# Performance work log

Hardware: AMD Instinct MI355X
Metric: run time of the kernel (lower is better)

The kernel has to match this reference:

```python
import jax, jax.numpy as jnp
import numpy as np
from jax.scipy.linalg import expm

B, Q, F, R, T, H = 2048, 16, 512, 400, 50, 256
STEPS = 100
DT = 1.0 / STEPS
COH = 50.0  # coherence_time


def setup_inputs() -> dict:
    ks = jax.random.split(jax.random.key(0), 48)
    it = iter(range(48))
    def rn(shape, s=1.0):
        return jax.random.normal(ks[next(it)], shape, dtype=jnp.float32) * s
    A = rn((Q, Q)); Bm = rn((Q, Q))
    d = {
        'molecular_features': rn((B, F)),
        'noise': rn((B, T, R), 0.1),          # torch.randn_like * 0.1
        'amp_re': rn((B, Q)), 'amp_im': rn((B, Q)),
        'H_re': (A + A.T) / 2.0,               # hermitized: real part symmetric
        'H_im': (Bm - Bm.T) / 2.0,             # imag part antisymmetric
        'gpc': rn((R,)),
        'bw1': rn((256, Q + F), (Q + F) ** -0.5), 'bb1': rn((256,), 0.01),
        'bw2': rn((128, 256), 256 ** -0.5), 'bb2': rn((128,), 0.01),
        'bw3': rn((R, 128), 128 ** -0.5), 'bb3': rn((R,), 0.01),
    }
    ins = [R, H, H]
    for l in range(3):
        d[f'Wih{l}'] = rn((4 * H, ins[l]), ins[l] ** -0.5)
        d[f'Whh{l}'] = rn((4 * H, H), H ** -0.5)
        d[f'bih{l}'] = rn((4 * H,), 0.01)
        d[f'bhh{l}'] = rn((4 * H,), 0.01)
    d.update({
        'cw1': rn((512, H + R), (H + R) ** -0.5), 'cb1': rn((512,), 0.01),
        'cw2': rn((256, 512), 512 ** -0.5), 'cb2': rn((256,), 0.01),
        'cw3': rn((64, 256), 256 ** -0.5), 'cb3': rn((64,), 0.01),
        'cw4': rn((1, 64), 64 ** -0.5), 'cb4': rn((1,), 0.01),
    })
    return d


def _lstm_layer(x, Wih, Whh, bih, bhh):
    # PyTorch LSTM gate order: i, f, g, o
    def step(carry, xt):
        h, c = carry
        z = xt @ Wih.T + h @ Whh.T + bih + bhh
        ig, fg, gg, og = jnp.split(z, 4, axis=-1)
        c = jax.nn.sigmoid(fg) * c + jax.nn.sigmoid(ig) * jnp.tanh(gg)
        h = jax.nn.sigmoid(og) * jnp.tanh(c)
        return (h, c), h
    n = x.shape[0]
    init = (jnp.zeros((n, H), x.dtype), jnp.zeros((n, H), x.dtype))
    (hT, _), hs = jax.lax.scan(step, init, jnp.swapaxes(x, 0, 1))
    return jnp.swapaxes(hs, 0, 1), hT


def _forward(molecular_features, noise, amp_re, amp_im, H_re, H_im, gpc,
             bw1, bb1, bw2, bb2, bw3, bb3,
             Wih0, Whh0, bih0, bhh0, Wih1, Whh1, bih1, bhh1, Wih2, Whh2, bih2, bhh2,
             cw1, cb1, cw2, cb2, cw3, cb3, cw4, cb4):
    Hp = (H_re + 1j * H_im).astype(jnp.complex64)
    amp = (amp_re + 1j * amp_im).astype(jnp.complex64)
    amp = amp / jnp.linalg.norm(amp, axis=-1, keepdims=True)  # F.normalize
    # molecular interaction Hamiltonian (real part only, as in source)
    M = jnp.einsum('bi,ij->bij', molecular_features[:, :Q], H_re)
    def qstep(a, step):
        t = step * DT
        Ht = Hp[None, :, :] + M * t                 # [B,Q,Q] complex
        U = jax.vmap(expm)(-1j * Ht * DT)           # per-sample matrix_exp
        a = jnp.einsum('bij,bj->bi', U, a) * jnp.exp(-t / COH)
        return a, None
    amp, _ = jax.lax.scan(qstep, amp, jnp.arange(STEPS, dtype=jnp.float32))
    obs = (jnp.abs(amp) ** 2).astype(jnp.float32)   # quantum observables
    bio = jnp.concatenate([obs, molecular_features], axis=-1)  # [B, Q+F]
    h1 = jax.nn.relu(bio @ bw1.T + bb1)
    h2 = jnp.tanh(h1 @ bw2.T + bb2)
    receptor = jax.nn.sigmoid(h2 @ bw3.T + bb3)     # [B, R]
    # biological signal transduction
    g_amp = receptor * jax.nn.sigmoid(gpc)
    adapt = jnp.exp(-jnp.arange(T, dtype=jnp.float32) / 10.0)[None, :, None]
    seq = g_amp[:, None, :] * adapt + noise         # [B, T, R]
    x, hT = _lstm_layer(seq, Wih0, Whh0, bih0, bhh0)
    x, hT = _lstm_layer(x, Wih1, Whh1, bih1, bhh1)
    x, hT = _lstm_layer(x, Wih2, Whh2, bih2, bhh2)  # hT: last-layer hidden [B,H]
    cf = jnp.concatenate([hT, receptor], axis=-1)   # [B, H+R]
    c1 = jax.nn.relu(cf @ cw1.T + cb1)
    c2 = jax.nn.relu(c1 @ cw2.T + cb2)
    c3 = jnp.tanh(c2 @ cw3.T + cb3)
    cons = jnp.mean(jax.nn.sigmoid(c3 @ cw4.T + cb4))
    valence = jnp.mean(jnp.tanh(x), axis=(1, 2))    # [B]
    return receptor, x, valence, cons, amp


def reference(molecular_features, noise, amp_re, amp_im, H_re, H_im, gpc,
              bw1, bb1, bw2, bb2, bw3, bb3,
              Wih0, Whh0, bih0, bhh0, Wih1, Whh1, bih1, bhh1, Wih2, Whh2, bih2, bhh2,
              cw1, cb1, cw2, cb2, cw3, cb3, cw4, cb4):
    receptor, seq, valence, cons, amp = _forward(
        molecular_features, noise, amp_re, amp_im, H_re, H_im, gpc,
        bw1, bb1, bw2, bb2, bw3, bb3,
        Wih0, Whh0, bih0, bhh0, Wih1, Whh1, bih1, bhh1, Wih2, Whh2, bih2, bhh2,
        cw1, cb1, cw2, cb2, cw3, cb3, cw4, cb4)
    # von Neumann entanglement entropy across a 2/2 qubit bipartition (Q=16 -> 4x4)
    half = 2 ** ((int(np.log2(Q))) // 2)
    rs = amp.reshape(amp.shape[0], half, -1)
    rho = jnp.einsum('bij,bik->bjk', rs, jnp.conj(rs))
    ev = jnp.clip(jnp.linalg.eigvals(rho).real, 1e-12, None)
    ent = jnp.mean(-jnp.sum(ev * jnp.log(ev), axis=-1))
    return receptor, seq, valence, cons, ent
```

## Files before the change

kernel.cpp:

```cpp
#include <hip/hip_runtime.h>
#include <stdint.h>


using short8 = __attribute__((ext_vector_type(8))) short;
using f32x4  = __attribute__((ext_vector_type(4))) float;

#define DEV static __device__ __forceinline__

typedef const __attribute__((address_space(1))) void GV;
typedef __attribute__((address_space(3))) void LV;
DEV void gload16(const void* g, void* l) {
  __builtin_amdgcn_global_load_lds((GV*)g, (LV*)l, 16, 0, 0);
}

DEV ushort f2b(float x) {
  union { float f; uint32_t u; } v; v.f = x;
  uint32_t r = v.u + 0x7FFFu + ((v.u >> 16) & 1u);
  return (ushort)(r >> 16);
}
DEV float b2f(ushort x) {
  union { uint32_t u; float f; } v; v.u = ((uint32_t)x) << 16; return v.f;
}
DEV float sigf(float x) { return 1.f / (1.f + __expf(-x)); }
DEV float tanh_fast(float x) {
  float xc = fminf(9.f, fmaxf(-9.f, x));
  float e = __expf(2.f * xc);
  return (e - 1.f) / (e + 1.f);
}

struct CJob { const float* src; ushort* dst; const float* scale;
              long n; int sr, sc, dc, mode; };
struct CJobs { CJob j[13]; };

__global__ __launch_bounds__(256)
void k_convbatch(CJobs jobs) {
  const int job = blockIdx.x >> 8;
  const int blk = blockIdx.x & 255;
  const CJob J = jobs.j[job];
  for (long idx = (long)blk * 256 + threadIdx.x; idx < J.n; idx += 256L * 256) {
    int r = (int)(idx / J.dc), c = (int)(idx % J.dc);
    float v = 0.f;
    if (r < J.sr && c < J.sc) {
      v = J.src[(long)r * J.sc + c];
      if (J.mode == 1) v *= sigf(J.scale[c]);
    }
    J.dst[idx] = f2b(v);
  }
}

__global__ __launch_bounds__(256)
void k_vadd3(const float* a0, const float* b0, const float* a1, const float* b1,
             const float* a2, const float* b2, float* o) {
  const int job = blockIdx.x >> 2;
  const int i = (blockIdx.x & 3) * 256 + threadIdx.x;
  const float* a = (job == 0) ? a0 : (job == 1) ? a1 : a2;
  const float* b = (job == 0) ? b0 : (job == 1) ? b1 : b2;
  o[job * 1024 + i] = a[i] + b[i];
}

__global__ __launch_bounds__(256)
void k_qb(const float* __restrict__ ampr_in, const float* __restrict__ ampi_in,
          const float* __restrict__ Hre, const float* __restrict__ Him,
          const float* __restrict__ mf, ushort* __restrict__ bio,
          float* __restrict__ ampr_out, float* __restrict__ ampi_out) {
  const int tid = threadIdx.x;
  if (blockIdx.x < 256) {
    const int gid = blockIdx.x * 256 + tid;
    const int b = gid >> 5;
    const int l32 = gid & 31;
    const int i = l32 & 15;
    const int h = l32 >> 4;
    float hre[8], him[8];
#pragma unroll
    for (int jj = 0; jj < 8; jj++) {
      hre[jj] = Hre[i * 16 + h * 8 + jj];
      him[jj] = Him[i * 16 + h * 8 + jj];
    }
    const float mfi = mf[(long)b * 512 + i];
    float are = ampr_in[b * 16 + i], aim = ampi_in[b * 16 + i];
    float ss = are * are + aim * aim;
#pragma unroll
    for (int m = 1; m < 32; m <<= 1) ss += __shfl_xor(ss, m, 32);
    ss *= 0.5f;
    const float inv = 1.f / sqrtf(ss);
    are *= inv; aim *= inv;
#pragma unroll 1
    for (int st = 0; st < 100; ++st) {
      const float t = (float)st * 0.01f;
      const float fac = 1.f + t * mfi;
      const float dec = __expf(-t * 0.02f);
      float tre = are, tim = aim, rre = are, rim = aim;
#pragma unroll 1
      for (int k = 1; k <= 5; k++) {
        float w1r = 0.f, w1i = 0.f, w2r = 0.f, w2i = 0.f;
#pragma unroll
        for (int jj = 0; jj < 8; jj++) {
          const float vr = __shfl(tre, h * 8 + jj, 32);
          const float vi = __shfl(tim, h * 8 + jj, 32);
          w1r += hre[jj] * vr; w1i += hre[jj] * vi;
          w2r += him[jj] * vr; w2i += him[jj] * vi;
        }
        w1r += __shfl_xor(w1r, 16, 32);
        w1i += __shfl_xor(w1i, 16, 32);
        w2r += __shfl_xor(w2r, 16, 32);
        w2i += __shfl_xor(w2i, 16, 32);
        const float hr = w1r * fac - w2i;
        const float hi = w1i * fac + w2r;
        const float sk = 0.01f / (float)k;
        tre = sk * hi; tim = -sk * hr;
        rre += tre; rim += tim;
      }
      are = rre * dec; aim = rim * dec;
    }
    if (h == 0) {
      ampr_out[b * 16 + i] = are;
      ampi_out[b * 16 + i] = aim;
      bio[(long)b * 576 + i] = f2b(are * are + aim * aim);
    }
  } else {
    for (long i = (long)(blockIdx.x - 256) * 256 + tid; i < (long)2048 * 512;
         i += 2048L * 256) {
      long b = i >> 9, k = i & 511;
      bio[b * 576 + 16 + k] = f2b(mf[i]);
    }
  }
}

template<int BT>
__global__ __launch_bounds__(256)
void k_gemm(const ushort* __restrict__ A, int lda,
            const ushort* __restrict__ W, int ldw,
            const float* __restrict__ bias,
            const ushort* __restrict__ Gg, int t0,
            float* __restrict__ Cf, int ldcf,
            ushort* __restrict__ Cb, int ldcb,
            int N, int K, int act, int swz) {
  constexpr int FR = BT / 32;
  constexpr int CH = BT / 32;
  __shared__ __align__(16) ushort lsA[2][BT * 64];
  __shared__ __align__(16) ushort lsB[2][BT * 64];
  const int tid = threadIdx.x;
  const int lane = tid & 63, w = tid >> 6;
  const int lr = lane & 15, lq = lane >> 4;
  const int wm = (w >> 1) * (BT / 2), wn = (w & 1) * (BT / 2);
  int bxb = blockIdx.x, byb = blockIdx.y;
  if (swz) {
    const int id = byb * gridDim.x + bxb;
    const int xcd = id & 7, q = id >> 3;
    byb = (q >> 4) * 16 + xcd * 2 + (q & 1);
    bxb = (q >> 1) & 7;
  }
  const int bm = byb * BT, bn = bxb * BT;
  const int srow = lane >> 3;
  const int scol = (((lane & 7) ^ srow)) * 8;

  auto stage = [&](int buf, int kk) {
#pragma unroll
    for (int c = 0; c < CH; c++) {
      const int ch = w * CH + c;
      const int r = ch * 8 + srow;
      gload16(A + (size_t)(bm + r) * lda + kk + scol, lsA[buf] + ch * 512);
      gload16(W + (size_t)(bn + r) * ldw + kk + scol, lsB[buf] + ch * 512);
    }
  };

  f32x4 acc[FR][FR];
#pragma unroll
  for (int i = 0; i < FR; i++)
#pragma unroll
    for (int j = 0; j < FR; j++) acc[i][j] = (f32x4){0.f, 0.f, 0.f, 0.f};

  stage(0, 0);
  __syncthreads();
  const int T = K >> 6;
  for (int t = 0; t < T; t++) {
    const int cur = t & 1;
    if (t + 1 < T) stage(cur ^ 1, (t + 1) * 64);
    short8 af[FR][2], bf[FR][2];
#pragma unroll
    for (int mi = 0; mi < FR; mi++)
#pragma unroll
      for (int k2 = 0; k2 < 2; k2++) {
        const int row = wm + mi * 16 + lr;
        af[mi][k2] = *(const short8*)(lsA[cur] + (row >> 3) * 512 + (row & 7) * 64 +
                                      (((k2 * 4 + lq) ^ (row & 7)) * 8));
      }
#pragma unroll
    for (int ni = 0; ni < FR; ni++)
#pragma unroll
      for (int k2 = 0; k2 < 2; k2++) {
        const int row = wn + ni * 16 + lr;
        bf[ni][k2] = *(const short8*)(lsB[cur] + (row >> 3) * 512 + (row & 7) * 64 +
                                      (((k2 * 4 + lq) ^ (row & 7)) * 8));
      }
#pragma unroll
    for (int k2 = 0; k2 < 2; k2++)
#pragma unroll
      for (int mi = 0; mi < FR; mi++)
#pragma unroll
        for (int ni = 0; ni < FR; ni++)
          acc[mi][ni] = __builtin_amdgcn_mfma_f32_16x16x32_bf16(
              af[mi][k2], bf[ni][k2], acc[mi][ni], 0, 0, 0);
    __syncthreads();
  }

#pragma unroll
  for (int mi = 0; mi < FR; mi++) {
#pragma unroll
    for (int r = 0; r < 4; r++) {
      const int row = bm + wm + mi * 16 + lq * 4 + r;
      float gfac = 0.f; const ushort* ggrow = nullptr;
      if (Gg) {
        gfac = __expf(-(float)(t0 + (row >> 11)) * 0.1f);
        ggrow = Gg + (size_t)(row & 2047) * 1024;
      }
#pragma unroll
      for (int ni = 0; ni < FR; ni++) {
        const int col = bn + wn + ni * 16 + lr;
        if (col < N) {
          float v = acc[mi][ni][r];
          if (bias) v += bias[col];
          if (Gg)  v += gfac * b2f(ggrow[col]);
          if (act == 1) v = fmaxf(v, 0.f);
          else if (act == 2) v = tanh_fast(v);
          else if (act == 3) v = sigf(v);
          if (Cf) Cf[(size_t)row * ldcf + col] = v;
          if (Cb) Cb[(size_t)row * ldcb + col] = f2b(v);
        }
      }
    }
  }
}

__global__ __launch_bounds__(512, 2)
void k_gemm8(const ushort* __restrict__ gA, int glda,
             const ushort* __restrict__ gW,
             const float* __restrict__ gbias, const ushort* __restrict__ gGg,
             int gt0, ushort* __restrict__ gC, int gK) {
  __shared__ __align__(16) ushort lsA[2 * 8192];
  __shared__ __align__(16) ushort lsB[2 * 8192];
  const int tid = threadIdx.x;
  const int gb = blockIdx.x;
  const int xcd = gb & 7, q = gb >> 3;
  const int byb = (q >> 4) * 16 + xcd * 2 + (q & 1);
  const int bxb = (q >> 1) & 7;
  const int bm = byb * 128, bn = bxb * 128;
  const int lane = tid & 63, wg = tid >> 6;
  const int lr = lane & 15, lq = lane >> 4;
  const int wm = (wg >> 2) * 64, wn = (wg & 3) * 32;
  const int srow = lane >> 3;
  const int scol = (((lane & 7) ^ srow)) * 8;

  f32x4 acc[4][2];
#pragma unroll
  for (int i = 0; i < 4; i++)
#pragma unroll
    for (int j = 0; j < 2; j++) acc[i][j] = (f32x4){0.f, 0.f, 0.f, 0.f};

#pragma unroll
  for (int c = 0; c < 2; c++) {
    const int ch = wg * 2 + c;
    const int r = ch * 8 + srow;
    gload16(gA + (size_t)(bm + r) * glda + scol, lsA + ch * 512);
    gload16(gW + (size_t)(bn + r) * glda + scol, lsB + ch * 512);
  }
  __syncthreads();

  const int T = gK >> 6;
  for (int t = 0; t < T; t++) {
    const int cur = t & 1;
    if (t + 1 < T) {
      const int kk = (t + 1) * 64;
#pragma unroll
      for (int c = 0; c < 2; c++) {
        const int ch = wg * 2 + c;
        const int r = ch * 8 + srow;
        gload16(gA + (size_t)(bm + r) * glda + kk + scol, lsA + (cur ^ 1) * 8192 + ch * 512);
        gload16(gW + (size_t)(bn + r) * glda + kk + scol, lsB + (cur ^ 1) * 8192 + ch * 512);
      }
    }
    {
      short8 af[4][2], bf[2][2];
#pragma unroll
      for (int mi = 0; mi < 4; mi++)
#pragma unroll
        for (int k2 = 0; k2 < 2; k2++) {
          const int row = wm + mi * 16 + lr;
          af[mi][k2] = *(const short8*)(lsA + cur * 8192 + (row >> 3) * 512 +
                                        (row & 7) * 64 + (((k2 * 4 + lq) ^ (row & 7)) * 8));
        }
#pragma unroll
      for (int ni = 0; ni < 2; ni++)
#pragma unroll
        for (int k2 = 0; k2 < 2; k2++) {
          const int row = wn + ni * 16 + lr;
          bf[ni][k2] = *(const short8*)(lsB + cur * 8192 + (row >> 3) * 512 +
                                        (row & 7) * 64 + (((k2 * 4 + lq) ^ (row & 7)) * 8));
        }
#pragma unroll
      for (int k2 = 0; k2 < 2; k2++)
#pragma unroll
        for (int mi = 0; mi < 4; mi++)
#pragma unroll
          for (int ni = 0; ni < 2; ni++)
            acc[mi][ni] = __builtin_amdgcn_mfma_f32_16x16x32_bf16(
                af[mi][k2], bf[ni][k2], acc[mi][ni], 0, 0, 0);
    }
    __syncthreads();
  }

#pragma unroll
  for (int mi = 0; mi < 4; mi++) {
#pragma unroll
    for (int r = 0; r < 4; r++) {
      const int row = bm + wm + mi * 16 + lq * 4 + r;
      float gfac = 0.f; const ushort* ggrow = nullptr;
      if (gGg) {
        gfac = __expf(-(float)(gt0 + (row >> 11)) * 0.1f);
        ggrow = gGg + (size_t)(row & 2047) * 1024;
      }
#pragma unroll
      for (int ni = 0; ni < 2; ni++) {
        const int col = bn + wn + ni * 16 + lr;
        float v = acc[mi][ni][r];
        if (gbias) v += gbias[col];
        if (gGg)  v += gfac * b2f(ggrow[col]);
        gC[(size_t)row * 1024 + col] = f2b(v);
      }
    }
  }
}

__global__ void k_noiseconv(const float* __restrict__ noise, ushort* __restrict__ dst, int t0) {
  long n = 10L * 2048 * 448;
  for (long idx = (long)blockIdx.x * blockDim.x + threadIdx.x; idx < n;
       idx += (long)gridDim.x * blockDim.x) {
    int r = (int)(idx % 448);
    long row = idx / 448;
    int b = (int)(row & 2047);
    int tl = (int)(row >> 11);
    ushort v = 0;
    if (r < 400)
      v = f2b(__builtin_nontemporal_load(&noise[((long)b * 50 + t0 + tl) * 400 + r]));
    dst[idx] = v;
  }
}

__global__ __launch_bounds__(512, 2)
void k_fused(const ushort* __restrict__ IH, const ushort* __restrict__ Whh,
             float* __restrict__ hstate, float* __restrict__ cstate,
             ushort* __restrict__ Hout, float* __restrict__ Xout, int t0,
             const ushort* __restrict__ gA, int glda,
             const ushort* __restrict__ gW,
             const float* __restrict__ gbias, const ushort* __restrict__ gGg,
             int gt0, ushort* __restrict__ gC, int gK) {
  __shared__ __align__(16) ushort upool[37024];
  const int tid = threadIdx.x;

  if (blockIdx.x < 128) {
    ushort (*h_lds)[266] = (ushort(*)[266])upool;
    ushort* ih0 = upool + 4256;
    const int lane = tid & 63, w8 = tid >> 6;
    const int lr = lane & 15, lq = lane >> 4;
    const int b0 = blockIdx.x * 16;
    const int wcols = w8 * 32;

    short8 wres[2][8];
#pragma unroll
    for (int cg = 0; cg < 2; cg++) {
      const ushort* wp = Whh + (size_t)(wcols + cg * 16 + lr) * 256 + lq * 8;
#pragma unroll
      for (int kk = 0; kk < 8; kk++) wres[cg][kk] = *(const short8*)(wp + kk * 32);
    }

    float c_reg[2][4], h_reg[2][4];
#pragma unroll
    for (int cg = 0; cg < 2; cg++) {
      const int j = wcols + cg * 16 + lr;
#pragma unroll
      for (int r = 0; r < 4; r++) {
        const int s = lq * 4 + r;
        float hv = hstate[(size_t)(b0 + s) * 256 + j];
        c_reg[cg][r] = cstate[(size_t)(b0 + s) * 256 + j];
        h_reg[cg][r] = hv;
        h_lds[s][j] = f2b(hv);
      }
    }
    __syncthreads();

#define LOADB(buf, g, cg) { \
  const ushort* wp_ = Whh + (size_t)((g) * 256 + wcols + (cg) * 16 + lr) * 256 + lq * 8; \
  _Pragma("unroll") for (int kk = 0; kk < 8; kk++) (buf)[kk] = *(const short8*)(wp_ + kk * 32); }
#define MFMAB(buf, g, cg) { \
  _Pragma("unroll") for (int kk = 0; kk < 8; kk++) \
    acc[cg][g] = __builtin_amdgcn_mfma_f32_16x16x32_bf16(af[kk], (buf)[kk], acc[cg][g], 0, 0, 0); }
#define MFMAR(cg) { \
  _Pragma("unroll") for (int kk = 0; kk < 8; kk++) \
    acc[cg][0] = __builtin_amdgcn_mfma_f32_16x16x32_bf16(af[kk], wres[cg][kk], acc[cg][0], 0, 0, 0); }

    for (int blk = 0; blk < 10; blk += 2) {
#pragma unroll
      for (int si = 0; si < 2; si++) {
        const ushort* src = IH + ((size_t)(blk + si) * 2048 + b0) * 1024;
#pragma unroll
        for (int u = 0; u < 4; u++) {
          const int bi = u * 8 + w8;
          gload16(src + (size_t)bi * 512 + lane * 8, ih0 + si * 16384 + bi * 512);
        }
      }
      __syncthreads();

      for (int i2 = 0; i2 < 2; i2++) {
        const int tl = blk + i2;
        const ushort* ihc = ih0 + i2 * 16384;
        short8 af[8];
#pragma unroll
        for (int kk = 0; kk < 8; kk++)
          af[kk] = *(const short8*)(&h_lds[lr][kk * 32 + lq * 8]);
        __syncthreads();

        f32x4 acc[2][4];
#pragma unroll
        for (int cg = 0; cg < 2; cg++)
#pragma unroll
          for (int g = 0; g < 4; g++) acc[cg][g] = (f32x4){0.f, 0.f, 0.f, 0.f};

        short8 wb0[8], wb1[8];
        LOADB(wb0, 1, 0);
        LOADB(wb1, 1, 1);
        MFMAR(0);
        MFMAR(1);
        MFMAB(wb0, 1, 0);
        LOADB(wb0, 2, 0);
        MFMAB(wb1, 1, 1);
        LOADB(wb1, 2, 1);
        MFMAB(wb0, 2, 0);
        LOADB(wb0, 3, 0);
        MFMAB(wb1, 2, 1);
        LOADB(wb1, 3, 1);
        MFMAB(wb0, 3, 0);
        MFMAB(wb1, 3, 1);

        const int t = t0 + tl;
#pragma unroll
        for (int cg = 0; cg < 2; cg++) {
          const int j = wcols + cg * 16 + lr;
#pragma unroll
          for (int r = 0; r < 4; r++) {
            const int s = lq * 4 + r;
            const float zi = acc[cg][0][r] + b2f(ihc[s * 1024 + j]);
            const float zf = acc[cg][1][r] + b2f(ihc[s * 1024 + 256 + j]);
            const float zg = acc[cg][2][r] + b2f(ihc[s * 1024 + 512 + j]);
            const float zo = acc[cg][3][r] + b2f(ihc[s * 1024 + 768 + j]);
            const float ig = sigf(zi), fg = sigf(zf), gg = tanh_fast(zg), og = sigf(zo);
            const float c = fg * c_reg[cg][r] + ig * gg;
            c_reg[cg][r] = c;
            const float h = og * tanh_fast(c);
            h_reg[cg][r] = h;
            h_lds[s][j] = f2b(h);
            if (Hout) Hout[((size_t)t * 2048 + b0 + s) * 256 + j] = f2b(h);
            if (Xout)
              __builtin_nontemporal_store(h, &Xout[((size_t)(b0 + s) * 50 + t) * 256 + j]);
          }
        }
        __syncthreads();
      }
    }
#undef LOADB
#undef MFMAB
#undef MFMAR
#pragma unroll
    for (int cg = 0; cg < 2; cg++) {
      const int j = wcols + cg * 16 + lr;
#pragma unroll
      for (int r = 0; r < 4; r++) {
        const int s = lq * 4 + r;
        hstate[(size_t)(b0 + s) * 256 + j] = h_reg[cg][r];
        cstate[(size_t)(b0 + s) * 256 + j] = c_reg[cg][r];
      }
    }
  } else {
    ushort* lsA = upool;
    ushort* lsB = upool + 16384;
    const int gb = blockIdx.x - 128;
    const int xcd = gb & 7, q = gb >> 3;
    const int byb = (q >> 4) * 16 + xcd * 2 + (q & 1);
    const int bxb = (q >> 1) & 7;
    const int bm = byb * 128, bn = bxb * 128;
    const int lane = tid & 63, wg = tid >> 6;
    const int lr = lane & 15, lq = lane >> 4;
    const int wm = (wg >> 2) * 64, wn = (wg & 3) * 32;
    const int srow = lane >> 3;
    const int scol = (((lane & 7) ^ srow)) * 8;

    f32x4 acc[4][2];
#pragma unroll
    for (int i = 0; i < 4; i++)
#pragma unroll
      for (int j = 0; j < 2; j++) acc[i][j] = (f32x4){0.f, 0.f, 0.f, 0.f};

#pragma unroll
    for (int c = 0; c < 2; c++) {
      const int ch = wg * 2 + c;
      const int r = ch * 8 + srow;
      gload16(gA + (size_t)(bm + r) * glda + scol, lsA + ch * 512);
      gload16(gW + (size_t)(bn + r) * glda + scol, lsB + ch * 512);
    }
    __syncthreads();

    const int T = gK >> 6;
    for (int t = 0; t < T; t++) {
      const int cur = t & 1;
      if (t + 1 < T) {
        const int kk = (t + 1) * 64;
#pragma unroll
        for (int c = 0; c < 2; c++) {
          const int ch = wg * 2 + c;
          const int r = ch * 8 + srow;
          gload16(gA + (size_t)(bm + r) * glda + kk + scol, lsA + (cur ^ 1) * 8192 + ch * 512);
          gload16(gW + (size_t)(bn + r) * glda + kk + scol, lsB + (cur ^ 1) * 8192 + ch * 512);
        }
      }
      {
        short8 af[4][2], bf[2][2];
#pragma unroll
        for (int mi = 0; mi < 4; mi++)
#pragma unroll
          for (int k2 = 0; k2 < 2; k2++) {
            const int row = wm + mi * 16 + lr;
            af[mi][k2] = *(const short8*)(lsA + cur * 8192 + (row >> 3) * 512 +
                                          (row & 7) * 64 + (((k2 * 4 + lq) ^ (row & 7)) * 8));
          }
#pragma unroll
        for (int ni = 0; ni < 2; ni++)
#pragma unroll
          for (int k2 = 0; k2 < 2; k2++) {
            const int row = wn + ni * 16 + lr;
            bf[ni][k2] = *(const short8*)(lsB + cur * 8192 + (row >> 3) * 512 +
                                          (row & 7) * 64 + (((k2 * 4 + lq) ^ (row & 7)) * 8));
          }
#pragma unroll
        for (int k2 = 0; k2 < 2; k2++)
#pragma unroll
          for (int mi = 0; mi < 4; mi++)
#pragma unroll
            for (int ni = 0; ni < 2; ni++)
              acc[mi][ni] = __builtin_amdgcn_mfma_f32_16x16x32_bf16(
                  af[mi][k2], bf[ni][k2], acc[mi][ni], 0, 0, 0);
      }
      __syncthreads();
    }

    {
#pragma unroll
      for (int mi = 0; mi < 4; mi++) {
#pragma unroll
        for (int r = 0; r < 4; r++) {
          const int row = bm + wm + mi * 16 + lq * 4 + r;
          float gfac = 0.f; const ushort* ggrow = nullptr;
          if (gGg) {
            gfac = __expf(-(float)(gt0 + (row >> 11)) * 0.1f);
            ggrow = gGg + (size_t)(row & 2047) * 1024;
          }
#pragma unroll
          for (int ni = 0; ni < 2; ni++) {
            const int col = bn + wn + ni * 16 + lr;
            float v = acc[mi][ni][r];
            if (gbias) v += gbias[col];
            if (gGg)  v += gfac * b2f(ggrow[col]);
            gC[(size_t)row * 1024 + col] = f2b(v);
          }
        }
      }
    }
  }
}

__global__ void k_cffill(const float* __restrict__ hT, const ushort* __restrict__ recb,
                         ushort* __restrict__ cf) {
  long i = (long)blockIdx.x * blockDim.x + threadIdx.x;
  if (i < (long)2048 * 656) {
    long b = i / 656; int c = (int)(i % 656);
    cf[b * 704 + c] = (c < 256) ? f2b(hT[b * 256 + c]) : recb[b * 448 + (c - 256)];
  }
}

__global__ __launch_bounds__(256)
void k_cons(const float* __restrict__ c3, const float* __restrict__ w4,
            const float* __restrict__ b4, float* __restrict__ out) {
  __shared__ float red[256];
  float accv = 0.f;
  for (int b = threadIdx.x; b < 2048; b += 256) {
    float d = b4[0];
#pragma unroll
    for (int k = 0; k < 64; k++) d += c3[(long)b * 64 + k] * w4[k];
    accv += sigf(d);
  }
  red[threadIdx.x] = accv; __syncthreads();
  for (int s = 128; s > 0; s >>= 1) {
    if (threadIdx.x < s) red[threadIdx.x] += red[threadIdx.x + s];
    __syncthreads();
  }
  if (threadIdx.x == 0) out[0] = red[0] * (1.f / 2048.f);
}

__global__ __launch_bounds__(256)
void k_val(const float* __restrict__ x, float* __restrict__ out) {
  __shared__ float red[256];
  const float* p = x + (size_t)blockIdx.x * 12800;
  float a = 0.f;
  for (int i = threadIdx.x; i < 12800; i += 256) a += tanh_fast(p[i]);
  red[threadIdx.x] = a; __syncthreads();
  for (int s = 128; s > 0; s >>= 1) {
    if (threadIdx.x < s) red[threadIdx.x] += red[threadIdx.x + s];
    __syncthreads();
  }
  if (threadIdx.x == 0) out[blockIdx.x] = red[0] * (1.f / 12800.f);
}

__global__ __launch_bounds__(64)
void k_ent(const float* __restrict__ ar, const float* __restrict__ ai,
           float* __restrict__ partial) {
  __shared__ float red[64];
  const int tid = threadIdx.x;
  const int b = blockIdx.x * 64 + tid;
  float vr[16], vi[16];
#pragma unroll
  for (int i = 0; i < 16; i++) { vr[i] = ar[b * 16 + i]; vi[i] = ai[b * 16 + i]; }
  float m[64];
#pragma unroll
  for (int j = 0; j < 4; j++)
#pragma unroll
    for (int k = 0; k < 4; k++) {
      float re = 0.f, im = 0.f;
#pragma unroll
      for (int i = 0; i < 4; i++) {
        float xr = vr[i * 4 + j], xi = vi[i * 4 + j];
        float yr = vr[i * 4 + k], yi = vi[i * 4 + k];
        re += xr * yr + xi * yi;
        im += xi * yr - xr * yi;
      }
      m[j * 8 + k] = re;
      m[j * 8 + (k + 4)] = -im;
      m[(j + 4) * 8 + k] = im;
      m[(j + 4) * 8 + (k + 4)] = re;
    }
#pragma unroll 1
  for (int sweep = 0; sweep < 6; ++sweep) {
#pragma unroll
    for (int p = 0; p < 7; p++) {
#pragma unroll
      for (int q = p + 1; q < 8; q++) {
        const float apq = m[p * 8 + q];
        if (fabsf(apq) > 1e-28f) {
          const float app = m[p * 8 + p], aqq = m[q * 8 + q];
          const float tau = (aqq - app) / (2.f * apq);
          const float tt = (tau >= 0.f ? 1.f : -1.f) /
                           (fabsf(tau) + sqrtf(1.f + tau * tau));
          const float cc = 1.f / sqrtf(1.f + tt * tt);
          const float ssn = tt * cc;
#pragma unroll
          for (int k2 = 0; k2 < 8; k2++) {
            const float mp = m[p * 8 + k2], mq = m[q * 8 + k2];
            m[p * 8 + k2] = cc * mp - ssn * mq;
            m[q * 8 + k2] = ssn * mp + cc * mq;
          }
#pragma unroll
          for (int k2 = 0; k2 < 8; k2++) {
            const float mp = m[k2 * 8 + p], mq = m[k2 * 8 + q];
            m[k2 * 8 + p] = cc * mp - ssn * mq;
            m[k2 * 8 + q] = ssn * mp + cc * mq;
          }
        }
      }
    }
  }
  float e = 0.f;
#pragma unroll
  for (int k2 = 0; k2 < 8; k2++) {
    const float lam = fmaxf(m[k2 * 8 + k2], 1e-12f);
    e -= lam * logf(lam);
  }
  red[tid] = e; __syncthreads();
  for (int s = 32; s > 0; s >>= 1) {
    if (tid < s) red[tid] += red[tid + s];
    __syncthreads();
  }
  if (tid == 0) partial[blockIdx.x] = red[0];
}

__global__ void k_entfin(const float* __restrict__ partial, float* __restrict__ out) {
  if (threadIdx.x == 0) {
    float s = 0.f;
    for (int i = 0; i < 32; i++) s += partial[i];
    out[0] = s * (0.5f / 2048.f);
  }
}

extern "C" void kernel_launch(void* const* d_in, const int* in_sizes, int n_in,
                              void* d_out, int out_size, void* d_ws, size_t ws_size,
                              hipStream_t stream) {
  (void)in_sizes; (void)n_in; (void)out_size; (void)ws_size;
  const float* mf    = (const float*)d_in[0];
  const float* noise = (const float*)d_in[1];
  const float* ampr  = (const float*)d_in[2];
  const float* ampi  = (const float*)d_in[3];
  const float* Hre   = (const float*)d_in[4];
  const float* Him   = (const float*)d_in[5];
  const float* gpc   = (const float*)d_in[6];
  const float* bw1 = (const float*)d_in[7];  const float* bb1 = (const float*)d_in[8];
  const float* bw2 = (const float*)d_in[9];  const float* bb2 = (const float*)d_in[10];
  const float* bw3 = (const float*)d_in[11]; const float* bb3 = (const float*)d_in[12];
  const float* Wih[3] = {(const float*)d_in[13], (const float*)d_in[17], (const float*)d_in[21]};
  const float* Whh[3] = {(const float*)d_in[14], (const float*)d_in[18], (const float*)d_in[22]};
  const float* bih[3] = {(const float*)d_in[15], (const float*)d_in[19], (const float*)d_in[23]};
  const float* bhh[3] = {(const float*)d_in[16], (const float*)d_in[20], (const float*)d_in[24]};
  const float* cw1 = (const float*)d_in[25]; const float* cb1 = (const float*)d_in[26];
  const float* cw2 = (const float*)d_in[27]; const float* cb2 = (const float*)d_in[28];
  const float* cw3 = (const float*)d_in[29]; const float* cb3 = (const float*)d_in[30];
  const float* cw4 = (const float*)d_in[31]; const float* cb4 = (const float*)d_in[32];

  float* out = (float*)d_out;
  float* out_rec  = out;
  float* out_seq  = out + 819200;
  float* out_val  = out + 27033600;
  float* out_cons = out + 27035648;
  float* out_ent  = out + 27035649;

  char* ws = (char*)d_ws;
  size_t off = 0;
  auto alloc = [&](size_t bytes) -> char* {
    char* p = ws + off; off += (bytes + 255) & ~(size_t)255; return p;
  };
  ushort* WB1   = (ushort*)alloc((size_t)256 * 576 * 2);
  ushort* WB2   = (ushort*)alloc((size_t)128 * 256 * 2);
  ushort* WB3   = (ushort*)alloc((size_t)512 * 128 * 2);
  ushort* WIH0  = (ushort*)alloc((size_t)1024 * 448 * 2);
  ushort* WIH0S = (ushort*)alloc((size_t)1024 * 448 * 2);
  ushort* WIH1  = (ushort*)alloc((size_t)1024 * 256 * 2);
  ushort* WIH2  = (ushort*)alloc((size_t)1024 * 256 * 2);
  ushort* WHH0  = (ushort*)alloc((size_t)1024 * 256 * 2);
  ushort* WHH1  = (ushort*)alloc((size_t)1024 * 256 * 2);
  ushort* WHH2  = (ushort*)alloc((size_t)1024 * 256 * 2);
  ushort* WC1   = (ushort*)alloc((size_t)512 * 704 * 2);
  ushort* WC2   = (ushort*)alloc((size_t)256 * 512 * 2);
  ushort* WC3   = (ushort*)alloc((size_t)128 * 256 * 2);
  float*  BSUM  = (float*)alloc((size_t)3 * 1024 * 4);
  ushort* BIO   = (ushort*)alloc((size_t)2048 * 576 * 2);
  ushort* H1B   = (ushort*)alloc((size_t)2048 * 256 * 2);
  ushort* H2B   = (ushort*)alloc((size_t)2048 * 128 * 2);
  ushort* RECB  = (ushort*)alloc((size_t)2048 * 448 * 2);
  ushort* GGB   = (ushort*)alloc((size_t)2048 * 1024 * 2);
  float*  AMPR  = (float*)alloc((size_t)2048 * 16 * 4);
  float*  AMPI  = (float*)alloc((size_t)2048 * 16 * 4);
  ushort* NCH   = (ushort*)alloc((size_t)10 * 2048 * 448 * 2);
  ushort* IHCA  = (ushort*)alloc((size_t)10 * 2048 * 1024 * 2);
  ushort* IHCB  = (ushort*)alloc((size_t)10 * 2048 * 1024 * 2);
  ushort* HBUF  = (ushort*)alloc((size_t)50 * 2048 * 256 * 2);
  float*  HST   = (float*)alloc((size_t)2048 * 256 * 4);
  float*  CST   = (float*)alloc((size_t)2048 * 256 * 4);
  ushort* CFB   = (ushort*)alloc((size_t)2048 * 704 * 2);
  ushort* C1B   = (ushort*)alloc((size_t)2048 * 512 * 2);
  ushort* C2B   = (ushort*)alloc((size_t)2048 * 256 * 2);
  float*  C3F   = (float*)alloc((size_t)2048 * 64 * 4);
  float*  ENTP  = (float*)alloc((size_t)32 * 4);

  hipMemsetAsync(BIO,  0, (size_t)2048 * 576 * 2, stream);
  hipMemsetAsync(RECB, 0, (size_t)2048 * 448 * 2, stream);
  hipMemsetAsync(CFB,  0, (size_t)2048 * 704 * 2, stream);

  CJobs cj;
  auto J = [&](int k, const float* s, ushort* d, int sr, int dr, int sc, int dc,
               const float* sc_, int mode) {
    cj.j[k] = CJob{s, d, sc_, (long)dr * dc, sr, sc, dc, mode};
  };
  J(0,  bw1,    WB1,   256, 256, 528, 576, nullptr, 0);
  J(1,  bw2,    WB2,   128, 128, 256, 256, nullptr, 0);
  J(2,  bw3,    WB3,   400, 512, 128, 128, nullptr, 0);
  J(3,  Wih[0], WIH0,  1024, 1024, 400, 448, nullptr, 0);
  J(4,  Wih[0], WIH0S, 1024, 1024, 400, 448, gpc, 1);
  J(5,  Wih[1], WIH1,  1024, 1024, 256, 256, nullptr, 0);
  J(6,  Wih[2], WIH2,  1024, 1024, 256, 256, nullptr, 0);
  J(7,  Whh[0], WHH0,  1024, 1024, 256, 256, nullptr, 0);
  J(8,  Whh[1], WHH1,  1024, 1024, 256, 256, nullptr, 0);
  J(9,  Whh[2], WHH2,  1024, 1024, 256, 256, nullptr, 0);
  J(10, cw1,    WC1,   512, 512, 656, 704, nullptr, 0);
  J(11, cw2,    WC2,   256, 256, 512, 512, nullptr, 0);
  J(12, cw3,    WC3,   64, 128, 256, 256, nullptr, 0);
  hipLaunchKernelGGL(k_convbatch, dim3(13 * 256), dim3(256), 0, stream, cj);
  hipLaunchKernelGGL(k_vadd3, dim3(12), dim3(256), 0, stream,
                     bih[0], bhh[0], bih[1], bhh[1], bih[2], bhh[2], BSUM);

  hipLaunchKernelGGL(k_qb, dim3(2304), dim3(256), 0, stream,
                     ampr, ampi, Hre, Him, mf, BIO, AMPR, AMPI);

  auto gemm = [&](bool big, const ushort* A, int lda, const ushort* W, int ldw,
                  const float* bias, const ushort* Gg, int t0, float* Cf, int ldcf,
                  ushort* Cb, int ldcb, int M, int N, int K, int act) {
    if (big) {
      dim3 grid((N + 127) / 128, M / 128);
      const int swz = (grid.x == 8 && (grid.y & 15) == 0) ? 1 : 0;
      hipLaunchKernelGGL(k_gemm<128>, grid, dim3(256), 0, stream,
                         A, lda, W, ldw, bias, Gg, t0, Cf, ldcf, Cb, ldcb, N, K, act, swz);
    } else {
      dim3 grid((N + 63) / 64, M / 64);
      hipLaunchKernelGGL(k_gemm<64>, grid, dim3(256), 0, stream,
                         A, lda, W, ldw, bias, Gg, t0, Cf, ldcf, Cb, ldcb, N, K, act, 0);
    }
  };

  gemm(false, BIO, 576, WB1, 576, bb1, nullptr, 0, nullptr, 0, H1B, 256, 2048, 256, 576, 1);
  gemm(false, H1B, 256, WB2, 256, bb2, nullptr, 0, nullptr, 0, H2B, 128, 2048, 128, 256, 2);
  gemm(false, H2B, 128, WB3, 128, bb3, nullptr, 0, out_rec, 400, RECB, 448, 2048, 400, 128, 3);
  gemm(false, RECB, 448, WIH0S, 448, nullptr, nullptr, 0, nullptr, 0, GGB, 1024, 2048, 1024, 448, 0);

  const ushort* WHHl[3] = {WHH0, WHH1, WHH2};
  ushort* IHCbuf[2] = {IHCA, IHCB};
  hipLaunchKernelGGL(k_noiseconv, dim3(8192), dim3(256), 0, stream, noise, NCH, 0);
  hipLaunchKernelGGL(k_gemm8, dim3(1280), dim3(512), 0, stream,
                     NCH, 448, WIH0, BSUM, GGB, 0, IHCA, 448);

  for (int i = 0; i < 15; i++) {
    const int l = i / 5, c = i % 5;
    if (c == 0) hipMemsetAsync(HST, 0, (size_t)2048 * 256 * 4 * 2, stream);
    const bool hg = (i + 1 < 15);
    const ushort* gA = nullptr; const ushort* gWp = nullptr;
    const float* gb_ = nullptr; const ushort* gGg = nullptr;
    int glda = 256, gK = 256, ggt0 = 0;
    if (hg) {
      const int l2 = (i + 1) / 5, c2 = (i + 1) % 5;
      if (l2 == 0) {
        hipLaunchKernelGGL(k_noiseconv, dim3(8192), dim3(256), 0, stream, noise, NCH, c2 * 10);
        gA = NCH; glda = 448; gK = 448; gb_ = BSUM; gGg = GGB; ggt0 = c2 * 10; gWp = WIH0;
      } else {
        gA = HBUF + (size_t)(c2 * 10) * 2048 * 256; glda = 256; gK = 256;
        gb_ = BSUM + l2 * 1024; gGg = nullptr; ggt0 = 0;
        gWp = (l2 == 1 ? WIH1 : WIH2);
      }
    }
    dim3 grid(hg ? 1408 : 128);
    hipLaunchKernelGGL(k_fused, grid, dim3(512), 0, stream,
                       IHCbuf[i & 1], WHHl[l], HST, CST,
                       (l < 2 ? HBUF : (ushort*)nullptr),
                       (l == 2 ? out_seq : (float*)nullptr), c * 10,
                       gA, glda, gWp, gb_, gGg, ggt0, IHCbuf[(i + 1) & 1], gK);
  }

  hipLaunchKernelGGL(k_cffill, dim3(5256), dim3(256), 0, stream, HST, RECB, CFB);
  gemm(false, CFB, 704, WC1, 704, cb1, nullptr, 0, nullptr, 0, C1B, 512, 2048, 512, 704, 1);
  gemm(false, C1B, 512, WC2, 512, cb2, nullptr, 0, nullptr, 0, C2B, 256, 2048, 256, 512, 1);
  gemm(false, C2B, 256, WC3, 256, cb3, nullptr, 0, C3F, 64, nullptr, 0, 2048, 64, 256, 2);
  hipLaunchKernelGGL(k_cons, dim3(1), dim3(256), 0, stream, C3F, cw4, cb4, out_cons);

  hipLaunchKernelGGL(k_val, dim3(2048), dim3(256), 0, stream, out_seq, out_val);
  hipLaunchKernelGGL(k_ent, dim3(32), dim3(64), 0, stream, AMPR, AMPI, ENTP);
  hipLaunchKernelGGL(k_entfin, dim3(1), dim3(32), 0, stream, ENTP, out_ent);
}
```

Measured before the change: 2.544 ms.

## Fold noise conversion into qb and fused LSTM kernels; merge tail kernels

Removes the standalone noise-to-bf16 conversion launches by converting the first two noise chunks inside k_qb and later chunks as extra blocks of k_fused, double-buffering the noise chunk buffer. The tail kernels (cf fill, valence, entropy) are merged into one launch, and cons with the entropy finish into another. This cuts kernel launches and lets the noise conversion overlap with recurrent LSTM work, at the cost of extra blocks competing with the latency-sensitive recurrent blocks and an extra noise buffer.

```diff
diff --git a/kernel.cpp b/kernel.cpp
--- a/kernel.cpp
+++ b/kernel.cpp
@@ -26,6 +26,21 @@
   float xc = fminf(9.f, fmaxf(-9.f, x));
   float e = __expf(2.f * xc);
   return (e - 1.f) / (e + 1.f);
+}
+
+DEV void noisecopy(const float* __restrict__ noise, ushort* __restrict__ dst,
+                   int t0, long start, long stride) {
+  const long n = 10L * 2048 * 448;
+  for (long idx = start; idx < n; idx += stride) {
+    int r = (int)(idx % 448);
+    long row = idx / 448;
+    int b = (int)(row & 2047);
+    int tl = (int)(row >> 11);
+    ushort v = 0;
+    if (r < 400)
+      v = f2b(__builtin_nontemporal_load(&noise[((long)b * 50 + t0 + tl) * 400 + r]));
+    dst[idx] = v;
+  }
 }
 
 struct CJob { const float* src; ushort* dst; const float* scale;
@@ -62,7 +77,9 @@
 void k_qb(const float* __restrict__ ampr_in, const float* __restrict__ ampi_in,
           const float* __restrict__ Hre, const float* __restrict__ Him,
           const float* __restrict__ mf, ushort* __restrict__ bio,
-          float* __restrict__ ampr_out, float* __restrict__ ampi_out) {
+          float* __restrict__ ampr_out, float* __restrict__ ampi_out,
+          const float* __restrict__ noise,
+          ushort* __restrict__ nch0, ushort* __restrict__ nch1) {
   const int tid = threadIdx.x;
   if (blockIdx.x < 256) {
     const int gid = blockIdx.x * 256 + tid;
@@ -117,12 +134,18 @@
       ampi_out[b * 16 + i] = aim;
       bio[(long)b * 576 + i] = f2b(are * are + aim * aim);
     }
-  } else {
+  } else if (blockIdx.x < 2304) {
     for (long i = (long)(blockIdx.x - 256) * 256 + tid; i < (long)2048 * 512;
          i += 2048L * 256) {
       long b = i >> 9, k = i & 511;
       bio[b * 576 + 16 + k] = f2b(mf[i]);
     }
+  } else {
+    const int cr = blockIdx.x - 2304;
+    const int half = cr >> 12;
+    const int blk = cr & 4095;
+    noisecopy(noise, half ? nch1 : nch0, half * 10,
+              (long)blk * 256 + tid, 4096L * 256);
   }
 }
 
@@ -331,21 +354,6 @@
   }
 }
 
-__global__ void k_noiseconv(const float* __restrict__ noise, ushort* __restrict__ dst, int t0) {
-  long n = 10L * 2048 * 448;
-  for (long idx = (long)blockIdx.x * blockDim.x + threadIdx.x; idx < n;
-       idx += (long)gridDim.x * blockDim.x) {
-    int r = (int)(idx % 448);
-    long row = idx / 448;
-    int b = (int)(row & 2047);
-    int tl = (int)(row >> 11);
-    ushort v = 0;
-    if (r < 400)
-      v = f2b(__builtin_nontemporal_load(&noise[((long)b * 50 + t0 + tl) * 400 + r]));
-    dst[idx] = v;
-  }
-}
-
 __global__ __launch_bounds__(512, 2)
 void k_fused(const ushort* __restrict__ IH, const ushort* __restrict__ Whh,
              float* __restrict__ hstate, float* __restrict__ cstate,
@@ -353,7 +361,9 @@
              const ushort* __restrict__ gA, int glda,
              const ushort* __restrict__ gW,
              const float* __restrict__ gbias, const ushort* __restrict__ gGg,
-             int gt0, ushort* __restrict__ gC, int gK) {
+             int gt0, ushort* __restrict__ gC, int gK,
+             const float* __restrict__ noise, ushort* __restrict__ ncdst,
+             int nct0) {
   __shared__ __align__(16) ushort upool[37024];
   const int tid = threadIdx.x;
 
@@ -479,7 +489,7 @@
         cstate[(size_t)(b0 + s) * 256 + j] = c_reg[cg][r];
       }
     }
-  } else {
+  } else if (blockIdx.x < 1408) {
     ushort* lsA = upool;
     ushort* lsB = upool + 16384;
     const int gb = blockIdx.x - 128;
@@ -573,127 +583,127 @@
         }
       }
     }
-  }
-}
-
-__global__ void k_cffill(const float* __restrict__ hT, const ushort* __restrict__ recb,
-                         ushort* __restrict__ cf) {
-  long i = (long)blockIdx.x * blockDim.x + threadIdx.x;
-  if (i < (long)2048 * 656) {
-    long b = i / 656; int c = (int)(i % 656);
-    cf[b * 704 + c] = (c < 256) ? f2b(hT[b * 256 + c]) : recb[b * 448 + (c - 256)];
+  } else {
+    const int blk = blockIdx.x - 1408;
+    noisecopy(noise, ncdst, nct0, (long)blk * 512 + tid, 2048L * 512);
   }
 }
 
 __global__ __launch_bounds__(256)
-void k_cons(const float* __restrict__ c3, const float* __restrict__ w4,
-            const float* __restrict__ b4, float* __restrict__ out) {
+void k_tail(const float* __restrict__ hT, const ushort* __restrict__ recb,
+            ushort* __restrict__ cf,
+            const float* __restrict__ x, float* __restrict__ valout,
+            const float* __restrict__ ar, const float* __restrict__ ai,
+            float* __restrict__ partial) {
   __shared__ float red[256];
-  float accv = 0.f;
-  for (int b = threadIdx.x; b < 2048; b += 256) {
-    float d = b4[0];
-#pragma unroll
-    for (int k = 0; k < 64; k++) d += c3[(long)b * 64 + k] * w4[k];
-    accv += sigf(d);
-  }
-  red[threadIdx.x] = accv; __syncthreads();
-  for (int s = 128; s > 0; s >>= 1) {
-    if (threadIdx.x < s) red[threadIdx.x] += red[threadIdx.x + s];
-    __syncthreads();
-  }
-  if (threadIdx.x == 0) out[0] = red[0] * (1.f / 2048.f);
+  const int tid = threadIdx.x;
+  if (blockIdx.x < 5256) {
+    long i = (long)blockIdx.x * 256 + tid;
+    if (i < (long)2048 * 656) {
+      long b = i / 656; int c = (int)(i % 656);
+      cf[b * 704 + c] = (c < 256) ? f2b(hT[b * 256 + c]) : recb[b * 448 + (c - 256)];
+    }
+  } else if (blockIdx.x < 7304) {
+    const float* p = x + (size_t)(blockIdx.x - 5256) * 12800;
+    float a = 0.f;
+    for (int i = tid; i < 12800; i += 256) a += tanh_fast(p[i]);
+    red[tid] = a; __syncthreads();
+    for (int s = 128; s > 0; s >>= 1) {
+      if (tid < s) red[tid] += red[tid + s];
+      __syncthreads();
+    }
+    if (tid == 0) valout[blockIdx.x - 5256] = red[0] * (1.f / 12800.f);
+  } else {
+    const int b = (blockIdx.x - 7304) * 256 + tid;
+    float vr[16], vi[16];
+#pragma unroll
+    for (int i = 0; i < 16; i++) { vr[i] = ar[b * 16 + i]; vi[i] = ai[b * 16 + i]; }
+    float m[64];
+#pragma unroll
+    for (int j = 0; j < 4; j++)
+#pragma unroll
+      for (int k = 0; k < 4; k++) {
+        float re = 0.f, im = 0.f;
+#pragma unroll
+        for (int i = 0; i < 4; i++) {
+          float xr = vr[i * 4 + j], xi = vi[i * 4 + j];
+          float yr = vr[i * 4 + k], yi = vi[i * 4 + k];
+          re += xr * yr + xi * yi;
+          im += xi * yr - xr * yi;
+        }
+        m[j * 8 + k] = re;
+        m[j * 8 + (k + 4)] = -im;
+        m[(j + 4) * 8 + k] = im;
+        m[(j + 4) * 8 + (k + 4)] = re;
+      }
+#pragma unroll 1
+    for (int sweep = 0; sweep < 6; ++sweep) {
+#pragma unroll
+      for (int p = 0; p < 7; p++) {
+#pragma unroll
+        for (int q = p + 1; q < 8; q++) {
+          const float apq = m[p * 8 + q];
+          if (fabsf(apq) > 1e-28f) {
+            const float app = m[p * 8 + p], aqq = m[q * 8 + q];
+            const float tau = (aqq - app) / (2.f * apq);
+            const float tt = (tau >= 0.f ? 1.f : -1.f) /
+                             (fabsf(tau) + sqrtf(1.f + tau * tau));
+            const float cc = 1.f / sqrtf(1.f + tt * tt);
+            const float ssn = tt * cc;
+#pragma unroll
+            for (int k2 = 0; k2 < 8; k2++) {
+              const float mp = m[p * 8 + k2], mq = m[q * 8 + k2];
+              m[p * 8 + k2] = cc * mp - ssn * mq;
+              m[q * 8 + k2] = ssn * mp + cc * mq;
+            }
+#pragma unroll
+            for (int k2 = 0; k2 < 8; k2++) {
+              const float mp = m[k2 * 8 + p], mq = m[k2 * 8 + q];
+              m[k2 * 8 + p] = cc * mp - ssn * mq;
+              m[k2 * 8 + q] = ssn * mp + cc * mq;
+            }
+          }
+        }
+      }
+    }
+    float e = 0.f;
+#pragma unroll
+    for (int k2 = 0; k2 < 8; k2++) {
+      const float lam = fmaxf(m[k2 * 8 + k2], 1e-12f);
+      e -= lam * logf(lam);
+    }
+    red[tid] = e; __syncthreads();
+    for (int s = 128; s > 0; s >>= 1) {
+      if (tid < s) red[tid] += red[tid + s];
+      __syncthreads();
+    }
+    if (tid == 0) partial[blockIdx.x - 7304] = red[0];
+  }
 }
 
 __global__ __launch_bounds__(256)
-void k_val(const float* __restrict__ x, float* __restrict__ out) {
-  __shared__ float red[256];
-  const float* p = x + (size_t)blockIdx.x * 12800;
-  float a = 0.f;
-  for (int i = threadIdx.x; i < 12800; i += 256) a += tanh_fast(p[i]);
-  red[threadIdx.x] = a; __syncthreads();
-  for (int s = 128; s > 0; s >>= 1) {
-    if (threadIdx.x < s) red[threadIdx.x] += red[threadIdx.x + s];
-    __syncthreads();
-  }
-  if (threadIdx.x == 0) out[blockIdx.x] = red[0] * (1.f / 12800.f);
-}
-
-__global__ __launch_bounds__(64)
-void k_ent(const float* __restrict__ ar, const float* __restrict__ ai,
-           float* __restrict__ partial) {
-  __shared__ float red[64];
-  const int tid = threadIdx.x;
-  const int b = blockIdx.x * 64 + tid;
-  float vr[16], vi[16];
-#pragma unroll
-  for (int i = 0; i < 16; i++) { vr[i] = ar[b * 16 + i]; vi[i] = ai[b * 16 + i]; }
-  float m[64];
-#pragma unroll
-  for (int j = 0; j < 4; j++)
-#pragma unroll
-    for (int k = 0; k < 4; k++) {
-      float re = 0.f, im = 0.f;
-#pragma unroll
-      for (int i = 0; i < 4; i++) {
-        float xr = vr[i * 4 + j], xi = vi[i * 4 + j];
-        float yr = vr[i * 4 + k], yi = vi[i * 4 + k];
-        re += xr * yr + xi * yi;
-        im += xi * yr - xr * yi;
-      }
-      m[j * 8 + k] = re;
-      m[j * 8 + (k + 4)] = -im;
-      m[(j + 4) * 8 + k] = im;
-      m[(j + 4) * 8 + (k + 4)] = re;
-    }
-#pragma unroll 1
-  for (int sweep = 0; sweep < 6; ++sweep) {
-#pragma unroll
-    for (int p = 0; p < 7; p++) {
-#pragma unroll
-      for (int q = p + 1; q < 8; q++) {
-        const float apq = m[p * 8 + q];
-        if (fabsf(apq) > 1e-28f) {
-          const float app = m[p * 8 + p], aqq = m[q * 8 + q];
-          const float tau = (aqq - app) / (2.f * apq);
-          const float tt = (tau >= 0.f ? 1.f : -1.f) /
-                           (fabsf(tau) + sqrtf(1.f + tau * tau));
-          const float cc = 1.f / sqrtf(1.f + tt * tt);
-          const float ssn = tt * cc;
-#pragma unroll
-          for (int k2 = 0; k2 < 8; k2++) {
-            const float mp = m[p * 8 + k2], mq = m[q * 8 + k2];
-            m[p * 8 + k2] = cc * mp - ssn * mq;
-            m[q * 8 + k2] = ssn * mp + cc * mq;
-          }
-#pragma unroll
-          for (int k2 = 0; k2 < 8; k2++) {
-            const float mp = m[k2 * 8 + p], mq = m[k2 * 8 + q];
-            m[k2 * 8 + p] = cc * mp - ssn * mq;
-            m[k2 * 8 + q] = ssn * mp + cc * mq;
-          }
-        }
-      }
-    }
-  }
-  float e = 0.f;
-#pragma unroll
-  for (int k2 = 0; k2 < 8; k2++) {
-    const float lam = fmaxf(m[k2 * 8 + k2], 1e-12f);
-    e -= lam * logf(lam);
-  }
-  red[tid] = e; __syncthreads();
-  for (int s = 32; s > 0; s >>= 1) {
-    if (tid < s) red[tid] += red[tid + s];
-    __syncthreads();
-  }
-  if (tid == 0) partial[blockIdx.x] = red[0];
-}
-
-__global__ void k_entfin(const float* __restrict__ partial, float* __restrict__ out) {
-  if (threadIdx.x == 0) {
+void k_consfin(const float* __restrict__ c3, const float* __restrict__ w4,
+               const float* __restrict__ b4, float* __restrict__ outc,
+               const float* __restrict__ partial, float* __restrict__ oute) {
+  if (blockIdx.x == 0) {
+    __shared__ float red[256];
+    float accv = 0.f;
+    for (int b = threadIdx.x; b < 2048; b += 256) {
+      float d = b4[0];
+#pragma unroll
+      for (int k = 0; k < 64; k++) d += c3[(long)b * 64 + k] * w4[k];
+      accv += sigf(d);
+    }
+    red[threadIdx.x] = accv; __syncthreads();
+    for (int s = 128; s > 0; s >>= 1) {
+      if (threadIdx.x < s) red[threadIdx.x] += red[threadIdx.x + s];
+      __syncthreads();
+    }
+    if (threadIdx.x == 0) outc[0] = red[0] * (1.f / 2048.f);
+  } else if (threadIdx.x == 0) {
     float s = 0.f;
-    for (int i = 0; i < 32; i++) s += partial[i];
-    out[0] = s * (0.5f / 2048.f);
+    for (int i = 0; i < 8; i++) s += partial[i];
+    oute[0] = s * (0.5f / 2048.f);
   }
 }
 
@@ -753,7 +763,8 @@
   ushort* GGB   = (ushort*)alloc((size_t)2048 * 1024 * 2);
   float*  AMPR  = (float*)alloc((size_t)2048 * 16 * 4);
   float*  AMPI  = (float*)alloc((size_t)2048 * 16 * 4);
-  ushort* NCH   = (ushort*)alloc((size_t)10 * 2048 * 448 * 2);
+  ushort* NCH0  = (ushort*)alloc((size_t)10 * 2048 * 448 * 2);
+  ushort* NCH1  = (ushort*)alloc((size_t)10 * 2048 * 448 * 2);
   ushort* IHCA  = (ushort*)alloc((size_t)10 * 2048 * 1024 * 2);
   ushort* IHCB  = (ushort*)alloc((size_t)10 * 2048 * 1024 * 2);
   ushort* HBUF  = (ushort*)alloc((size_t)50 * 2048 * 256 * 2);
@@ -763,7 +774,7 @@
   ushort* C1B   = (ushort*)alloc((size_t)2048 * 512 * 2);
   ushort* C2B   = (ushort*)alloc((size_t)2048 * 256 * 2);
   float*  C3F   = (float*)alloc((size_t)2048 * 64 * 4);
-  float*  ENTP  = (float*)alloc((size_t)32 * 4);
+  float*  ENTP  = (float*)alloc((size_t)8 * 4);
 
   hipMemsetAsync(BIO,  0, (size_t)2048 * 576 * 2, stream);
   hipMemsetAsync(RECB, 0, (size_t)2048 * 448 * 2, stream);
@@ -791,8 +802,9 @@
   hipLaunchKernelGGL(k_vadd3, dim3(12), dim3(256), 0, stream,
                      bih[0], bhh[0], bih[1], bhh[1], bih[2], bhh[2], BSUM);
 
-  hipLaunchKernelGGL(k_qb, dim3(2304), dim3(256), 0, stream,
-                     ampr, ampi, Hre, Him, mf, BIO, AMPR, AMPI);
+  hipLaunchKernelGGL(k_qb, dim3(10496), dim3(256), 0, stream,
+                     ampr, ampi, Hre, Him, mf, BIO, AMPR, AMPI,
+                     noise, NCH0, NCH1);
 
   auto gemm = [&](bool big, const ushort* A, int lda, const ushort* W, int ldw,
                   const float* bias, const ushort* Gg, int t0, float* Cf, int ldcf,
@@ -816,43 +828,43 @@
 
   const ushort* WHHl[3] = {WHH0, WHH1, WHH2};
   ushort* IHCbuf[2] = {IHCA, IHCB};
-  hipLaunchKernelGGL(k_noiseconv, dim3(8192), dim3(256), 0, stream, noise, NCH, 0);
+  ushort* NCHbuf[2] = {NCH0, NCH1};
   hipLaunchKernelGGL(k_gemm8, dim3(1280), dim3(512), 0, stream,
-                     NCH, 448, WIH0, BSUM, GGB, 0, IHCA, 448);
+                     NCH0, 448, WIH0, BSUM, GGB, 0, IHCA, 448);
 
   for (int i = 0; i < 15; i++) {
     const int l = i / 5, c = i % 5;
     if (c == 0) hipMemsetAsync(HST, 0, (size_t)2048 * 256 * 4 * 2, stream);
     const bool hg = (i + 1 < 15);
+    const bool hc = (i <= 2);
     const ushort* gA = nullptr; const ushort* gWp = nullptr;
     const float* gb_ = nullptr; const ushort* gGg = nullptr;
     int glda = 256, gK = 256, ggt0 = 0;
     if (hg) {
       const int l2 = (i + 1) / 5, c2 = (i + 1) % 5;
       if (l2 == 0) {
-        hipLaunchKernelGGL(k_noiseconv, dim3(8192), dim3(256), 0, stream, noise, NCH, c2 * 10);
-        gA = NCH; glda = 448; gK = 448; gb_ = BSUM; gGg = GGB; ggt0 = c2 * 10; gWp = WIH0;
+        gA = NCHbuf[(i + 1) & 1]; glda = 448; gK = 448;
+        gb_ = BSUM; gGg = GGB; ggt0 = c2 * 10; gWp = WIH0;
       } else {
         gA = HBUF + (size_t)(c2 * 10) * 2048 * 256; glda = 256; gK = 256;
         gb_ = BSUM + l2 * 1024; gGg = nullptr; ggt0 = 0;
         gWp = (l2 == 1 ? WIH1 : WIH2);
       }
     }
-    dim3 grid(hg ? 1408 : 128);
+    dim3 grid(hg ? (hc ? 3456 : 1408) : 128);
     hipLaunchKernelGGL(k_fused, grid, dim3(512), 0, stream,
                        IHCbuf[i & 1], WHHl[l], HST, CST,
                        (l < 2 ? HBUF : (ushort*)nullptr),
                        (l == 2 ? out_seq : (float*)nullptr), c * 10,
-                       gA, glda, gWp, gb_, gGg, ggt0, IHCbuf[(i + 1) & 1], gK);
-  }
-
-  hipLaunchKernelGGL(k_cffill, dim3(5256), dim3(256), 0, stream, HST, RECB, CFB);
+                       gA, glda, gWp, gb_, gGg, ggt0, IHCbuf[(i + 1) & 1], gK,
+                       noise, hc ? NCHbuf[i & 1] : (ushort*)nullptr, (i + 2) * 10);
+  }
+
+  hipLaunchKernelGGL(k_tail, dim3(7312), dim3(256), 0, stream,
+                     HST, RECB, CFB, out_seq, out_val, AMPR, AMPI, ENTP);
   gemm(false, CFB, 704, WC1, 704, cb1, nullptr, 0, nullptr, 0, C1B, 512, 2048, 512, 704, 1);
   gemm(false, C1B, 512, WC2, 512, cb2, nullptr, 0, nullptr, 0, C2B, 256, 2048, 256, 512, 1);
   gemm(false, C2B, 256, WC3, 256, cb3, nullptr, 0, C3F, 64, nullptr, 0, 2048, 64, 256, 2);
-  hipLaunchKernelGGL(k_cons, dim3(1), dim3(256), 0, stream, C3F, cw4, cb4, out_cons);
-
-  hipLaunchKernelGGL(k_val, dim3(2048), dim3(256), 0, stream, out_seq, out_val);
-  hipLaunchKernelGGL(k_ent, dim3(32), dim3(64), 0, stream, AMPR, AMPI, ENTP);
-  hipLaunchKernelGGL(k_entfin, dim3(1), dim3(32), 0, stream, ENTP, out_ent);
-}
+  hipLaunchKernelGGL(k_consfin, dim3(2), dim3(256), 0, stream,
+                     C3F, cw4, cb4, out_cons, ENTP, out_ent);
+}
```

Result: slower. 2.599 ms (+2.2%).
